# Optimization experiments

Measured on AMD Instinct MI355X. Metric: run time of the kernel, lower is better.

## Reference

```python
import jax, jax.numpy as jnp
import numpy as np

OUT = 7          # output_size
SR = 2           # sampling_ratio
CANON_SIZE = 224.0
CANON_LVL = 4
MIN_LVL, MAX_LVL = 2, 5
SCALES = (0.25, 0.125, 0.0625, 0.03125)
IMG = 1024.0


def _roi_align(feat, batch_idx, boxes, scale):
    """ROIAlign aligned=True. feat [B,C,H,W], boxes [R,4] (x1,y1,x2,y2) in image coords.
    Returns [R,C,OUT,OUT]."""
    B, C, H, W = feat.shape
    R = boxes.shape[0]
    x1 = boxes[:, 0] * scale - 0.5
    y1 = boxes[:, 1] * scale - 0.5
    x2 = boxes[:, 2] * scale - 0.5
    y2 = boxes[:, 3] * scale - 0.5
    bin_w = (x2 - x1) / OUT
    bin_h = (y2 - y1) / OUT
    S = OUT * SR
    # sample positions in bin units: bin p, sub-sample i -> p + (i+0.5)/SR
    g = (jnp.arange(S, dtype=feat.dtype) + 0.5) / SR
    ys = y1[:, None] + g[None, :] * bin_h[:, None]   # [R,S]
    xs = x1[:, None] + g[None, :] * bin_w[:, None]   # [R,S]
    vy = (ys >= -1.0) & (ys <= H)
    vx = (xs >= -1.0) & (xs <= W)
    yc = jnp.clip(ys, 0.0, H - 1)
    xc = jnp.clip(xs, 0.0, W - 1)
    y0 = jnp.floor(yc).astype(jnp.int32)
    x0 = jnp.floor(xc).astype(jnp.int32)
    y1i = jnp.minimum(y0 + 1, H - 1)
    x1i = jnp.minimum(x0 + 1, W - 1)
    ly = yc - y0.astype(feat.dtype); hy = 1.0 - ly
    lx = xc - x0.astype(feat.dtype); hx = 1.0 - lx
    f = jnp.transpose(feat, (0, 2, 3, 1))            # [B,H,W,C]
    b = batch_idx[:, None, None]                     # [R,1,1]

    def gather(yi, xi):
        # advanced indexing broadcast -> [R,S,S,C]
        return f[b, yi[:, :, None], xi[:, None, :], :]

    def w2(wy, wx):
        return (wy[:, :, None] * wx[:, None, :])[..., None]

    v = (gather(y0, x0) * w2(hy, hx)
         + gather(y0, x1i) * w2(hy, lx)
         + gather(y1i, x0) * w2(ly, hx)
         + gather(y1i, x1i) * w2(ly, lx))             # [R,S,S,C]
    mask = (vy[:, :, None] & vx[:, None, :])[..., None]
    v = jnp.where(mask, v, jnp.zeros((), feat.dtype))
    v = v.reshape(R, OUT, SR, OUT, SR, C).mean(axis=(2, 4))  # avg over SRxSR samples
    return jnp.transpose(v, (0, 3, 1, 2))            # [R,C,OUT,OUT]


def setup_inputs() -> dict:
    key = jax.random.key(0)
    k2, k3, k4, k5, kwh, kc = jax.random.split(key, 6)
    B, C, N = 2, 256, 256
    x2 = jax.random.normal(k2, (B, C, 256, 256), jnp.float32)
    x3 = jax.random.normal(k3, (B, C, 128, 128), jnp.float32)
    x4 = jax.random.normal(k4, (B, C, 64, 64), jnp.float32)
    x5 = jax.random.normal(k5, (B, C, 32, 32), jnp.float32)
    wh = jax.random.uniform(kwh, (B, N, 2), jnp.float32, 32.0, 480.0)
    cxy = jax.random.uniform(kc, (B, N, 2), jnp.float32, 0.0, IMG)
    p1 = jnp.clip(cxy - wh / 2, 0.0, IMG)
    p2 = jnp.clip(cxy + wh / 2, 0.0, IMG)
    boxes = jnp.concatenate([p1, p2], axis=-1)  # [B,N,4] = (x1,y1,x2,y2)
    return {"x2": x2, "x3": x3, "x4": x4, "x5": x5, "boxes": boxes}


def reference(x2, x3, x4, x5, boxes):
    B, N, _ = boxes.shape
    flat = boxes.reshape(B * N, 4)
    batch_idx = jnp.repeat(jnp.arange(B, dtype=jnp.int32), N)
    # FPN level assignment
    area = (flat[:, 2] - flat[:, 0]) * (flat[:, 3] - flat[:, 1])
    sizes = jnp.sqrt(area)
    lvl = jnp.floor(CANON_LVL + jnp.log2(sizes / CANON_SIZE + 1e-8))
    lvl = jnp.clip(lvl, MIN_LVL, MAX_LVL).astype(jnp.int32) - MIN_LVL  # [R] in {0..3}
    feats = (x2, x3, x4, x5)
    C = x2.shape[1]
    out = jnp.zeros((B * N, C, OUT, OUT), x2.dtype)
    for l, (f, s) in enumerate(zip(feats, SCALES)):
        pooled = _roi_align(f, batch_idx, flat, s)
        out = jnp.where((lvl == l)[:, None, None, None], pooled, out)
    return out
```

## Files before the change

kernel.cpp:

```cpp
#include <hip/hip_runtime.h>


#define OUTD 7
#define CCH  256
#define NBOX 256
#define NC   4
#define NCHK (CCH / NC)
#define CAPU 300
#define CAPF (CAPU * 4)
#define NBIN (OUTD * OUTD)

typedef __attribute__((address_space(1))) unsigned int gu32;
typedef __attribute__((address_space(3))) unsigned int lu32;

__device__ __forceinline__ void gl2lds16(const float* g, float* l) {
    __builtin_amdgcn_global_load_lds((gu32*)(unsigned long long)g, (lu32*)l, 16, 0, 0);
}

__global__ __launch_bounds__(256) void roi_direct(
    const float* __restrict__ f0, const float* __restrict__ f1,
    const float* __restrict__ f2, const float* __restrict__ f3,
    const float* __restrict__ boxes, float* __restrict__ out)
{
    const int roi = blockIdx.x;
    const int t   = threadIdx.x;
    const int wv  = t >> 6;
    const int ln  = t & 63;
    const int c   = blockIdx.y * NC + wv;
    const int b   = roi >> 8;

    const float bx1 = boxes[roi * 4 + 0];
    const float by1 = boxes[roi * 4 + 1];
    const float bx2 = boxes[roi * 4 + 2];
    const float by2 = boxes[roi * 4 + 3];

    const float area = (bx2 - bx1) * (by2 - by1);
    const float sz   = sqrtf(area);
    int lvl = (int)floorf(4.0f + log2f(sz * (1.0f / 224.0f) + 1e-8f));
    lvl = min(max(lvl, 2), 5) - 2;

    const int   wsh   = 8 - lvl;
    const int   H     = 1 << wsh;
    const int   W     = H;
    const float scale = 1.0f / (float)(4 << lvl);
    const float* f = (lvl == 0) ? f0 : (lvl == 1) ? f1 : (lvl == 2) ? f2 : f3;

    const float x1r = bx1 * scale - 0.5f;
    const float y1r = by1 * scale - 0.5f;
    const float bw  = (bx2 - bx1) * scale * (1.0f / OUTD);
    const float bh  = (by2 - by1) * scale * (1.0f / OUTD);
    const float Wm1 = (float)(W - 1);

    const int xf = (int)fminf(fmaxf(x1r + 0.25f * bw, 0.0f), Wm1);
    const int yf = (int)fminf(fmaxf(y1r + 0.25f * bh, 0.0f), Wm1);
    const int xl = min((int)fminf(fmaxf(x1r + 6.75f * bw, 0.0f), Wm1) + 1, W - 1);
    const int yl = min((int)fminf(fmaxf(y1r + 6.75f * bh, 0.0f), Wm1) + 1, W - 1);
    const int x_lo = xf & ~3;
    const int y_lo = yf;
    const int W4 = (xl - x_lo + 4) >> 2;
    const int Hw = yl - y_lo + 1;
    const int L4 = Hw * W4;
    const int rs = W4 << 2;

    __shared__ __align__(16) float s_win[NC * CAPF];

    const bool fast = (L4 <= CAPU);

    const unsigned int cbase = ((unsigned int)(b * CCH + c)) << (2 * wsh);
    if (fast) {
        const unsigned int wbase = ((unsigned int)y_lo << wsh) + (unsigned int)x_lo;
        const unsigned int gmax  = (512u << (2 * wsh)) - 4u;
        const float invW4 = 1.0f / (float)W4;
        float* lb = s_win + wv * CAPF;
        for (int o0 = 0; o0 < L4; o0 += 64) {
            const int u = o0 + ln;
            if (u < L4) {
                int y  = (int)((float)u * invW4);
                int x4 = u - y * W4;
                if (x4 < 0) { x4 += W4; --y; } else if (x4 >= W4) { x4 -= W4; ++y; }
                unsigned int g = cbase + wbase + ((unsigned int)y << wsh) + ((unsigned int)x4 << 2);
                g = min(g, gmax);
                gl2lds16(f + g, lb + (o0 << 2));
            }
        }
    }

    const int l  = min(ln, 48);
    const int oy = l / 7;
    const int ox = l - oy * 7;

    const float ysA = y1r + ((float)(2 * oy) + 0.5f) * 0.5f * bh;
    const float ysB = y1r + ((float)(2 * oy + 1) + 0.5f) * 0.5f * bh;
    const float xsA = x1r + ((float)(2 * ox) + 0.5f) * 0.5f * bw;
    const float xsB = x1r + ((float)(2 * ox + 1) + 0.5f) * 0.5f * bw;

    const float vyA = ((ysA >= -1.0f) && (ysA <= (float)H)) ? 1.0f : 0.0f;
    const float vyB = ((ysB >= -1.0f) && (ysB <= (float)H)) ? 1.0f : 0.0f;
    const float vxA = ((xsA >= -1.0f) && (xsA <= (float)W)) ? 1.0f : 0.0f;
    const float vxB = ((xsB >= -1.0f) && (xsB <= (float)W)) ? 1.0f : 0.0f;

    const float ycA = fminf(fmaxf(ysA, 0.0f), Wm1);
    const float ycB = fminf(fmaxf(ysB, 0.0f), Wm1);
    const float xcA = fminf(fmaxf(xsA, 0.0f), Wm1);
    const float xcB = fminf(fmaxf(xsB, 0.0f), Wm1);

    const int yA0 = (int)ycA, yB0 = (int)ycB;
    const int xA0 = (int)xcA, xB0 = (int)xcB;
    const int yA1 = min(yA0 + 1, H - 1), yB1 = min(yB0 + 1, H - 1);
    const int xA1 = min(xA0 + 1, W - 1), xB1 = min(xB0 + 1, W - 1);

    const float lyA = ycA - (float)yA0, lyB = ycB - (float)yB0;
    const float lxA = xcA - (float)xA0, lxB = xcB - (float)xB0;

    const float wyAh = vyA * (1.0f - lyA), wyAl = vyA * lyA;
    const float wyBh = vyB * (1.0f - lyB), wyBl = vyB * lyB;
    const float wxAh = vxA * (1.0f - lxA), wxAl = vxA * lxA;
    const float wxBh = vxB * (1.0f - lxB), wxBl = vxB * lxB;

    float acc;
    if (fast) {
        const int ryA0 = (yA0 - y_lo) * rs, ryA1 = (yA1 - y_lo) * rs;
        const int ryB0 = (yB0 - y_lo) * rs, ryB1 = (yB1 - y_lo) * rs;
        const int rxA0 = xA0 - x_lo, rxA1 = xA1 - x_lo;
        const int rxB0 = xB0 - x_lo, rxB1 = xB1 - x_lo;

        asm volatile("s_waitcnt vmcnt(0)" ::: "memory");
        __builtin_amdgcn_sched_barrier(0);

        const float* w = s_win + wv * CAPF;
        acc =
            wyAh * (wxAh * w[ryA0 + rxA0] + wxAl * w[ryA0 + rxA1])
          + wyAl * (wxAh * w[ryA1 + rxA0] + wxAl * w[ryA1 + rxA1])
          + wyAh * (wxBh * w[ryA0 + rxB0] + wxBl * w[ryA0 + rxB1])
          + wyAl * (wxBh * w[ryA1 + rxB0] + wxBl * w[ryA1 + rxB1])
          + wyBh * (wxAh * w[ryB0 + rxA0] + wxAl * w[ryB0 + rxA1])
          + wyBl * (wxAh * w[ryB1 + rxA0] + wxAl * w[ryB1 + rxA1])
          + wyBh * (wxBh * w[ryB0 + rxB0] + wxBl * w[ryB0 + rxB1])
          + wyBl * (wxBh * w[ryB1 + rxB0] + wxBl * w[ryB1 + rxB1]);
    } else {
        const float* fc = f + cbase;
        const int gA0 = yA0 << wsh, gA1 = yA1 << wsh;
        const int gB0 = yB0 << wsh, gB1 = yB1 << wsh;
        acc =
            wyAh * (wxAh * fc[gA0 + xA0] + wxAl * fc[gA0 + xA1])
          + wyAl * (wxAh * fc[gA1 + xA0] + wxAl * fc[gA1 + xA1])
          + wyAh * (wxBh * fc[gA0 + xB0] + wxBl * fc[gA0 + xB1])
          + wyAl * (wxBh * fc[gA1 + xB0] + wxBl * fc[gA1 + xB1])
          + wyBh * (wxAh * fc[gB0 + xA0] + wxAl * fc[gB0 + xA1])
          + wyBl * (wxAh * fc[gB1 + xA0] + wxAl * fc[gB1 + xA1])
          + wyBh * (wxBh * fc[gB0 + xB0] + wxBl * fc[gB0 + xB1])
          + wyBl * (wxBh * fc[gB1 + xB0] + wxBl * fc[gB1 + xB1]);
    }

    if (ln < NBIN) {
        out[(size_t)roi * (CCH * NBIN) + (size_t)c * NBIN + ln] = acc * 0.25f;
    }
}

extern "C" void kernel_launch(void* const* d_in, const int* in_sizes, int n_in,
                              void* d_out, int out_size, void* d_ws, size_t ws_size,
                              hipStream_t stream) {
    const float* f0    = (const float*)d_in[0];
    const float* f1    = (const float*)d_in[1];
    const float* f2    = (const float*)d_in[2];
    const float* f3    = (const float*)d_in[3];
    const float* boxes = (const float*)d_in[4];
    float*       outp  = (float*)d_out;

    const int R = out_size / (CCH * NBIN);
    roi_direct<<<dim3(R, NCHK), 256, 0, stream>>>(f0, f1, f2, f3, boxes, outp);
}
```

Measured before the change: 260.0 us.

## Precompute per-ROI sampling geometry in setup kernel and process two channels per wave

Adds a small setup kernel that computes each ROI's level, window bounds, bilinear indices, weights and per-load window offsets once, and writes them to workspace. The main kernel reads these tables instead of redoing the per-thread geometry and divisions for every channel block. Each wave now handles two channels with the loads issued together, and the grid is reordered so channel blocks of one ROI run close together. This costs an extra launch, a workspace dependency with a fallback kernel, and odd nroi inference logic.

After: 245.3 us. 5.6% less time.

```diff
diff --git a/kernel.cpp b/kernel.cpp
--- a/kernel.cpp
+++ b/kernel.cpp
@@ -4,11 +4,14 @@
 #define OUTD 7
 #define CCH  256
 #define NBOX 256
-#define NC   4
-#define NCHK (CCH / NC)
+#define NBIN 49
 #define CAPU 300
 #define CAPF (CAPU * 4)
-#define NBIN (OUTD * OUTD)
+
+#define NC   8
+#define NCHK (CCH / NC)
+
+#define WS_STRIDE 1280
 
 typedef __attribute__((address_space(1))) unsigned int gu32;
 typedef __attribute__((address_space(3))) unsigned int lu32;
@@ -17,7 +20,213 @@
     __builtin_amdgcn_global_load_lds((gu32*)(unsigned long long)g, (lu32*)l, 16, 0, 0);
 }
 
-__global__ __launch_bounds__(256) void roi_direct(
+struct Geo {
+    int wsh, W, H; float x1r, y1r, bw, bh, Wm1;
+    int x_lo, y_lo, W4, Hw, L4, rs;
+};
+
+__device__ __forceinline__ Geo mkgeo(float bx1, float by1, float bx2, float by2) {
+    Geo g;
+    const float area = (bx2 - bx1) * (by2 - by1);
+    const float sz   = sqrtf(area);
+    int lvl = (int)floorf(4.0f + log2f(sz * (1.0f / 224.0f) + 1e-8f));
+    lvl = min(max(lvl, 2), 5) - 2;
+    g.wsh = 8 - lvl; g.W = 1 << g.wsh; g.H = g.W;
+    const float scale = 1.0f / (float)(4 << lvl);
+    g.x1r = bx1 * scale - 0.5f;
+    g.y1r = by1 * scale - 0.5f;
+    g.bw  = (bx2 - bx1) * scale * (1.0f / OUTD);
+    g.bh  = (by2 - by1) * scale * (1.0f / OUTD);
+    g.Wm1 = (float)(g.W - 1);
+    const int xf = (int)fminf(fmaxf(g.x1r + 0.25f * g.bw, 0.0f), g.Wm1);
+    const int yf = (int)fminf(fmaxf(g.y1r + 0.25f * g.bh, 0.0f), g.Wm1);
+    const int xl = min((int)fminf(fmaxf(g.x1r + 6.75f * g.bw, 0.0f), g.Wm1) + 1, g.W - 1);
+    const int yl = min((int)fminf(fmaxf(g.y1r + 6.75f * g.bh, 0.0f), g.Wm1) + 1, g.W - 1);
+    g.x_lo = xf & ~3;
+    g.y_lo = yf;
+    g.W4 = (xl - g.x_lo + 4) >> 2;
+    g.Hw = yl - g.y_lo + 1;
+    g.L4 = g.Hw * g.W4;
+    g.rs = g.W4 << 2;
+    return g;
+}
+
+__global__ __launch_bounds__(64) void roi_setup(const float* __restrict__ boxes,
+                                                unsigned char* __restrict__ ws)
+{
+    const int roi = blockIdx.x;
+    const int ln  = threadIdx.x;
+    const Geo g = mkgeo(boxes[roi * 4 + 0], boxes[roi * 4 + 1],
+                        boxes[roi * 4 + 2], boxes[roi * 4 + 3]);
+    const int b = roi >> 8;
+    unsigned char* wr = ws + (size_t)roi * WS_STRIDE;
+
+    if (ln == 0) {
+        unsigned int* hdr = (unsigned int*)wr;
+        hdr[0] = (unsigned int)g.wsh;
+        hdr[1] = ((unsigned int)(b * CCH) << (2 * g.wsh))
+               + ((unsigned int)g.y_lo << g.wsh) + (unsigned int)g.x_lo;
+        hdr[2] = (unsigned int)g.W4;
+        hdr[3] = (unsigned int)g.L4;
+        hdr[4] = (unsigned int)g.rs;
+        hdr[5] = (512u << (2 * g.wsh)) - 4u;
+    }
+    if (ln < 14) {
+        const float gg = ((float)ln + 0.5f) * 0.5f;
+        const float ys = g.y1r + gg * g.bh;
+        const float xs = g.x1r + gg * g.bw;
+        const float vy = ((ys >= -1.0f) && (ys <= (float)g.H)) ? 1.0f : 0.0f;
+        const float vx = ((xs >= -1.0f) && (xs <= (float)g.W)) ? 1.0f : 0.0f;
+        const float yc = fminf(fmaxf(ys, 0.0f), g.Wm1);
+        const float xc = fminf(fmaxf(xs, 0.0f), g.Wm1);
+        const int y0 = (int)yc, x0 = (int)xc;
+        const int y1 = min(y0 + 1, g.H - 1), x1 = min(x0 + 1, g.W - 1);
+        const float ly = yc - (float)y0, lx = xc - (float)x0;
+        ((int2*)  (wr + 32 ))[ln] = make_int2((y0 - g.y_lo) * g.rs, (y1 - g.y_lo) * g.rs);
+        ((float2*)(wr + 144))[ln] = make_float2(vy * (1.0f - ly), vy * ly);
+        ((int2*)  (wr + 256))[ln] = make_int2(x0 - g.x_lo, x1 - g.x_lo);
+        ((float2*)(wr + 368))[ln] = make_float2(vx * (1.0f - lx), vx * lx);
+    }
+    unsigned short* offs = (unsigned short*)(wr + 480);
+    const int nU = min(g.L4, 304);
+    const float invW4 = 1.0f / (float)g.W4;
+    for (int u = ln; u < nU; u += 64) {
+        int y  = (int)((float)u * invW4);
+        int x4 = u - y * g.W4;
+        if (x4 < 0) { x4 += g.W4; --y; } else if (x4 >= g.W4) { x4 -= g.W4; ++y; }
+        offs[u] = (unsigned short)((y << (g.wsh - 2)) + x4);
+    }
+}
+
+__global__ __launch_bounds__(256) void roi_main(
+    const float* __restrict__ f0, const float* __restrict__ f1,
+    const float* __restrict__ f2, const float* __restrict__ f3,
+    const float* __restrict__ boxes,
+    const unsigned char* __restrict__ ws, float* __restrict__ out)
+{
+    const int roi = blockIdx.y;
+    const int c0  = blockIdx.x * NC;
+    const int t   = threadIdx.x;
+    const int wv  = t >> 6;
+    const int ln  = t & 63;
+
+    const unsigned char* wr  = ws + (size_t)roi * WS_STRIDE;
+    const unsigned int*  hdr = (const unsigned int*)wr;
+    const unsigned int wsh = hdr[0], ubase = hdr[1];
+    const unsigned int L4  = hdr[3], gmax  = hdr[5];
+
+    const int lvl = 8 - (int)wsh;
+    const float* f = (lvl == 0) ? f0 : (lvl == 1) ? f1 : (lvl == 2) ? f2 : f3;
+
+    const int l  = min(ln, 48);
+    const int oy = l / 7;
+    const int ox = l - oy * 7;
+
+    const int4   ypk = *(const int4*)  (wr + 32  + 16 * oy);
+    const float4 wyp = *(const float4*)(wr + 144 + 16 * oy);
+    const int4   xpk = *(const int4*)  (wr + 256 + 16 * ox);
+    const float4 wxp = *(const float4*)(wr + 368 + 16 * ox);
+
+    const int ca = c0 + wv;
+    const int cb = c0 + wv + 4;
+    const size_t obase = (size_t)roi * (CCH * NBIN);
+
+    __shared__ __align__(16) float s_win[NC * CAPF];
+
+    if (L4 <= CAPU) {
+        const unsigned short* offs = (const unsigned short*)(wr + 480);
+        unsigned int rel[5];
+        #pragma unroll
+        for (int k = 0; k < 5; ++k)
+            rel[k] = ((unsigned int)offs[min(ln + (k << 6), (int)L4 - 1)]) << 2;
+
+        float* sa = s_win + wv * CAPF;
+        float* sb = s_win + (wv + 4) * CAPF;
+        const unsigned int cba = ubase + ((unsigned int)ca << (2 * wsh));
+        const unsigned int cbb = ubase + ((unsigned int)cb << (2 * wsh));
+        #pragma unroll
+        for (int k = 0; k < 5; ++k)
+            if (ln + (k << 6) < (int)L4)
+                gl2lds16(f + min(cba + rel[k], gmax), sa + (k << 8));
+        #pragma unroll
+        for (int k = 0; k < 5; ++k)
+            if (ln + (k << 6) < (int)L4)
+                gl2lds16(f + min(cbb + rel[k], gmax), sb + (k << 8));
+
+        asm volatile("s_waitcnt vmcnt(0)" ::: "memory");
+        __builtin_amdgcn_sched_barrier(0);
+
+        const float accA =
+            wyp.x * (wxp.x * sa[ypk.x + xpk.x] + wxp.y * sa[ypk.x + xpk.y])
+          + wyp.y * (wxp.x * sa[ypk.y + xpk.x] + wxp.y * sa[ypk.y + xpk.y])
+          + wyp.x * (wxp.z * sa[ypk.x + xpk.z] + wxp.w * sa[ypk.x + xpk.w])
+          + wyp.y * (wxp.z * sa[ypk.y + xpk.z] + wxp.w * sa[ypk.y + xpk.w])
+          + wyp.z * (wxp.x * sa[ypk.z + xpk.x] + wxp.y * sa[ypk.z + xpk.y])
+          + wyp.w * (wxp.x * sa[ypk.w + xpk.x] + wxp.y * sa[ypk.w + xpk.y])
+          + wyp.z * (wxp.z * sa[ypk.z + xpk.z] + wxp.w * sa[ypk.z + xpk.w])
+          + wyp.w * (wxp.z * sa[ypk.w + xpk.z] + wxp.w * sa[ypk.w + xpk.w]);
+        const float accB =
+            wyp.x * (wxp.x * sb[ypk.x + xpk.x] + wxp.y * sb[ypk.x + xpk.y])
+          + wyp.y * (wxp.x * sb[ypk.y + xpk.x] + wxp.y * sb[ypk.y + xpk.y])
+          + wyp.x * (wxp.z * sb[ypk.x + xpk.z] + wxp.w * sb[ypk.x + xpk.w])
+          + wyp.y * (wxp.z * sb[ypk.y + xpk.z] + wxp.w * sb[ypk.y + xpk.w])
+          + wyp.z * (wxp.x * sb[ypk.z + xpk.x] + wxp.y * sb[ypk.z + xpk.y])
+          + wyp.w * (wxp.x * sb[ypk.w + xpk.x] + wxp.y * sb[ypk.w + xpk.y])
+          + wyp.z * (wxp.z * sb[ypk.z + xpk.z] + wxp.w * sb[ypk.z + xpk.w])
+          + wyp.w * (wxp.z * sb[ypk.w + xpk.z] + wxp.w * sb[ypk.w + xpk.w]);
+
+        if (ln < NBIN) {
+            out[obase + (size_t)ca * NBIN + ln] = accA * 0.25f;
+            out[obase + (size_t)cb * NBIN + ln] = accB * 0.25f;
+        }
+    } else {
+        const Geo g = mkgeo(boxes[roi * 4 + 0], boxes[roi * 4 + 1],
+                            boxes[roi * 4 + 2], boxes[roi * 4 + 3]);
+        const float ysA = g.y1r + ((float)(2 * oy) + 0.5f) * 0.5f * g.bh;
+        const float ysB = g.y1r + ((float)(2 * oy + 1) + 0.5f) * 0.5f * g.bh;
+        const float xsA = g.x1r + ((float)(2 * ox) + 0.5f) * 0.5f * g.bw;
+        const float xsB = g.x1r + ((float)(2 * ox + 1) + 0.5f) * 0.5f * g.bw;
+        const float vyA = ((ysA >= -1.0f) && (ysA <= (float)g.H)) ? 1.0f : 0.0f;
+        const float vyB = ((ysB >= -1.0f) && (ysB <= (float)g.H)) ? 1.0f : 0.0f;
+        const float vxA = ((xsA >= -1.0f) && (xsA <= (float)g.W)) ? 1.0f : 0.0f;
+        const float vxB = ((xsB >= -1.0f) && (xsB <= (float)g.W)) ? 1.0f : 0.0f;
+        const float ycA = fminf(fmaxf(ysA, 0.0f), g.Wm1);
+        const float ycB = fminf(fmaxf(ysB, 0.0f), g.Wm1);
+        const float xcA = fminf(fmaxf(xsA, 0.0f), g.Wm1);
+        const float xcB = fminf(fmaxf(xsB, 0.0f), g.Wm1);
+        const int yA0 = (int)ycA, yB0 = (int)ycB, xA0 = (int)xcA, xB0 = (int)xcB;
+        const int yA1 = min(yA0 + 1, g.H - 1), yB1 = min(yB0 + 1, g.H - 1);
+        const int xA1 = min(xA0 + 1, g.W - 1), xB1 = min(xB0 + 1, g.W - 1);
+        const float lyA = ycA - (float)yA0, lyB = ycB - (float)yB0;
+        const float lxA = xcA - (float)xA0, lxB = xcB - (float)xB0;
+        const float wyAh = vyA * (1.0f - lyA), wyAl = vyA * lyA;
+        const float wyBh = vyB * (1.0f - lyB), wyBl = vyB * lyB;
+        const float wxAh = vxA * (1.0f - lxA), wxAl = vxA * lxA;
+        const float wxBh = vxB * (1.0f - lxB), wxBl = vxB * lxB;
+        const int gA0 = yA0 << g.wsh, gA1 = yA1 << g.wsh;
+        const int gB0 = yB0 << g.wsh, gB1 = yB1 << g.wsh;
+        const int b = roi >> 8;
+        #pragma unroll
+        for (int s = 0; s < 2; ++s) {
+            const int c = s ? cb : ca;
+            const float* fc = f + (((size_t)(b * CCH + c)) << (2 * g.wsh));
+            const float acc =
+                wyAh * (wxAh * fc[gA0 + xA0] + wxAl * fc[gA0 + xA1])
+              + wyAl * (wxAh * fc[gA1 + xA0] + wxAl * fc[gA1 + xA1])
+              + wyAh * (wxBh * fc[gA0 + xB0] + wxBl * fc[gA0 + xB1])
+              + wyAl * (wxBh * fc[gA1 + xB0] + wxBl * fc[gA1 + xB1])
+              + wyBh * (wxAh * fc[gB0 + xA0] + wxAl * fc[gB0 + xA1])
+              + wyBl * (wxAh * fc[gB1 + xA0] + wxAl * fc[gB1 + xA1])
+              + wyBh * (wxBh * fc[gB0 + xB0] + wxBl * fc[gB0 + xB1])
+              + wyBl * (wxBh * fc[gB1 + xB0] + wxBl * fc[gB1 + xB1]);
+            if (ln < NBIN)
+                out[obase + (size_t)c * NBIN + ln] = acc * 0.25f;
+        }
+    }
+}
+
+#define MNC 4
+__global__ __launch_bounds__(256) void roi_mono(
     const float* __restrict__ f0, const float* __restrict__ f1,
     const float* __restrict__ f2, const float* __restrict__ f3,
     const float* __restrict__ boxes, float* __restrict__ out)
@@ -26,61 +235,31 @@
     const int t   = threadIdx.x;
     const int wv  = t >> 6;
     const int ln  = t & 63;
-    const int c   = blockIdx.y * NC + wv;
+    const int c   = blockIdx.y * MNC + wv;
     const int b   = roi >> 8;
 
-    const float bx1 = boxes[roi * 4 + 0];
-    const float by1 = boxes[roi * 4 + 1];
-    const float bx2 = boxes[roi * 4 + 2];
-    const float by2 = boxes[roi * 4 + 3];
-
-    const float area = (bx2 - bx1) * (by2 - by1);
-    const float sz   = sqrtf(area);
-    int lvl = (int)floorf(4.0f + log2f(sz * (1.0f / 224.0f) + 1e-8f));
-    lvl = min(max(lvl, 2), 5) - 2;
-
-    const int   wsh   = 8 - lvl;
-    const int   H     = 1 << wsh;
-    const int   W     = H;
-    const float scale = 1.0f / (float)(4 << lvl);
+    const Geo g = mkgeo(boxes[roi * 4 + 0], boxes[roi * 4 + 1],
+                        boxes[roi * 4 + 2], boxes[roi * 4 + 3]);
+    const int lvl = 8 - g.wsh;
     const float* f = (lvl == 0) ? f0 : (lvl == 1) ? f1 : (lvl == 2) ? f2 : f3;
 
-    const float x1r = bx1 * scale - 0.5f;
-    const float y1r = by1 * scale - 0.5f;
-    const float bw  = (bx2 - bx1) * scale * (1.0f / OUTD);
-    const float bh  = (by2 - by1) * scale * (1.0f / OUTD);
-    const float Wm1 = (float)(W - 1);
-
-    const int xf = (int)fminf(fmaxf(x1r + 0.25f * bw, 0.0f), Wm1);
-    const int yf = (int)fminf(fmaxf(y1r + 0.25f * bh, 0.0f), Wm1);
-    const int xl = min((int)fminf(fmaxf(x1r + 6.75f * bw, 0.0f), Wm1) + 1, W - 1);
-    const int yl = min((int)fminf(fmaxf(y1r + 6.75f * bh, 0.0f), Wm1) + 1, W - 1);
-    const int x_lo = xf & ~3;
-    const int y_lo = yf;
-    const int W4 = (xl - x_lo + 4) >> 2;
-    const int Hw = yl - y_lo + 1;
-    const int L4 = Hw * W4;
-    const int rs = W4 << 2;
-
-    __shared__ __align__(16) float s_win[NC * CAPF];
-
-    const bool fast = (L4 <= CAPU);
-
-    const unsigned int cbase = ((unsigned int)(b * CCH + c)) << (2 * wsh);
+    __shared__ __align__(16) float s_win[MNC * CAPF];
+    const bool fast = (g.L4 <= CAPU);
+    const unsigned int cbase = ((unsigned int)(b * CCH + c)) << (2 * g.wsh);
+
     if (fast) {
-        const unsigned int wbase = ((unsigned int)y_lo << wsh) + (unsigned int)x_lo;
-        const unsigned int gmax  = (512u << (2 * wsh)) - 4u;
-        const float invW4 = 1.0f / (float)W4;
+        const unsigned int wbase = ((unsigned int)g.y_lo << g.wsh) + (unsigned int)g.x_lo;
+        const unsigned int gmax  = (512u << (2 * g.wsh)) - 4u;
+        const float invW4 = 1.0f / (float)g.W4;
         float* lb = s_win + wv * CAPF;
-        for (int o0 = 0; o0 < L4; o0 += 64) {
+        for (int o0 = 0; o0 < g.L4; o0 += 64) {
             const int u = o0 + ln;
-            if (u < L4) {
+            if (u < g.L4) {
                 int y  = (int)((float)u * invW4);
-                int x4 = u - y * W4;
-                if (x4 < 0) { x4 += W4; --y; } else if (x4 >= W4) { x4 -= W4; ++y; }
-                unsigned int g = cbase + wbase + ((unsigned int)y << wsh) + ((unsigned int)x4 << 2);
-                g = min(g, gmax);
-                gl2lds16(f + g, lb + (o0 << 2));
+                int x4 = u - y * g.W4;
+                if (x4 < 0) { x4 += g.W4; --y; } else if (x4 >= g.W4) { x4 -= g.W4; ++y; }
+                unsigned int gg = cbase + wbase + ((unsigned int)y << g.wsh) + ((unsigned int)x4 << 2);
+                gl2lds16(f + min(gg, gmax), lb + (o0 << 2));
             }
         }
     }
@@ -88,30 +267,23 @@
     const int l  = min(ln, 48);
     const int oy = l / 7;
     const int ox = l - oy * 7;
-
-    const float ysA = y1r + ((float)(2 * oy) + 0.5f) * 0.5f * bh;
-    const float ysB = y1r + ((float)(2 * oy + 1) + 0.5f) * 0.5f * bh;
-    const float xsA = x1r + ((float)(2 * ox) + 0.5f) * 0.5f * bw;
-    const float xsB = x1r + ((float)(2 * ox + 1) + 0.5f) * 0.5f * bw;
-
-    const float vyA = ((ysA >= -1.0f) && (ysA <= (float)H)) ? 1.0f : 0.0f;
-    const float vyB = ((ysB >= -1.0f) && (ysB <= (float)H)) ? 1.0f : 0.0f;
-    const float vxA = ((xsA >= -1.0f) && (xsA <= (float)W)) ? 1.0f : 0.0f;
-    const float vxB = ((xsB >= -1.0f) && (xsB <= (float)W)) ? 1.0f : 0.0f;
-
-    const float ycA = fminf(fmaxf(ysA, 0.0f), Wm1);
-    const float ycB = fminf(fmaxf(ysB, 0.0f), Wm1);
-    const float xcA = fminf(fmaxf(xsA, 0.0f), Wm1);
-    const float xcB = fminf(fmaxf(xsB, 0.0f), Wm1);
-
-    const int yA0 = (int)ycA, yB0 = (int)ycB;
-    const int xA0 = (int)xcA, xB0 = (int)xcB;
-    const int yA1 = min(yA0 + 1, H - 1), yB1 = min(yB0 + 1, H - 1);
-    const int xA1 = min(xA0 + 1, W - 1), xB1 = min(xB0 + 1, W - 1);
-
+    const float ysA = g.y1r + ((float)(2 * oy) + 0.5f) * 0.5f * g.bh;
+    const float ysB = g.y1r + ((float)(2 * oy + 1) + 0.5f) * 0.5f * g.bh;
+    const float xsA = g.x1r + ((float)(2 * ox) + 0.5f) * 0.5f * g.bw;
+    const float xsB = g.x1r + ((float)(2 * ox + 1) + 0.5f) * 0.5f * g.bw;
+    const float vyA = ((ysA >= -1.0f) && (ysA <= (float)g.H)) ? 1.0f : 0.0f;
+    const float vyB = ((ysB >= -1.0f) && (ysB <= (float)g.H)) ? 1.0f : 0.0f;
+    const float vxA = ((xsA >= -1.0f) && (xsA <= (float)g.W)) ? 1.0f : 0.0f;
+    const float vxB = ((xsB >= -1.0f) && (xsB <= (float)g.W)) ? 1.0f : 0.0f;
+    const float ycA = fminf(fmaxf(ysA, 0.0f), g.Wm1);
+    const float ycB = fminf(fmaxf(ysB, 0.0f), g.Wm1);
+    const float xcA = fminf(fmaxf(xsA, 0.0f), g.Wm1);
+    const float xcB = fminf(fmaxf(xsB, 0.0f), g.Wm1);
+    const int yA0 = (int)ycA, yB0 = (int)ycB, xA0 = (int)xcA, xB0 = (int)xcB;
+    const int yA1 = min(yA0 + 1, g.H - 1), yB1 = min(yB0 + 1, g.H - 1);
+    const int xA1 = min(xA0 + 1, g.W - 1), xB1 = min(xB0 + 1, g.W - 1);
     const float lyA = ycA - (float)yA0, lyB = ycB - (float)yB0;
     const float lxA = xcA - (float)xA0, lxB = xcB - (float)xB0;
-
     const float wyAh = vyA * (1.0f - lyA), wyAl = vyA * lyA;
     const float wyBh = vyB * (1.0f - lyB), wyBl = vyB * lyB;
     const float wxAh = vxA * (1.0f - lxA), wxAl = vxA * lxA;
@@ -119,14 +291,12 @@
 
     float acc;
     if (fast) {
-        const int ryA0 = (yA0 - y_lo) * rs, ryA1 = (yA1 - y_lo) * rs;
-        const int ryB0 = (yB0 - y_lo) * rs, ryB1 = (yB1 - y_lo) * rs;
-        const int rxA0 = xA0 - x_lo, rxA1 = xA1 - x_lo;
-        const int rxB0 = xB0 - x_lo, rxB1 = xB1 - x_lo;
-
+        const int ryA0 = (yA0 - g.y_lo) * g.rs, ryA1 = (yA1 - g.y_lo) * g.rs;
+        const int ryB0 = (yB0 - g.y_lo) * g.rs, ryB1 = (yB1 - g.y_lo) * g.rs;
+        const int rxA0 = xA0 - g.x_lo, rxA1 = xA1 - g.x_lo;
+        const int rxB0 = xB0 - g.x_lo, rxB1 = xB1 - g.x_lo;
         asm volatile("s_waitcnt vmcnt(0)" ::: "memory");
         __builtin_amdgcn_sched_barrier(0);
-
         const float* w = s_win + wv * CAPF;
         acc =
             wyAh * (wxAh * w[ryA0 + rxA0] + wxAl * w[ryA0 + rxA1])
@@ -139,8 +309,8 @@
           + wyBl * (wxBh * w[ryB1 + rxB0] + wxBl * w[ryB1 + rxB1]);
     } else {
         const float* fc = f + cbase;
-        const int gA0 = yA0 << wsh, gA1 = yA1 << wsh;
-        const int gB0 = yB0 << wsh, gB1 = yB1 << wsh;
+        const int gA0 = yA0 << g.wsh, gA1 = yA1 << g.wsh;
+        const int gB0 = yB0 << g.wsh, gB1 = yB1 << g.wsh;
         acc =
             wyAh * (wxAh * fc[gA0 + xA0] + wxAl * fc[gA0 + xA1])
           + wyAl * (wxAh * fc[gA1 + xA0] + wxAl * fc[gA1 + xA1])
@@ -167,6 +337,15 @@
     const float* boxes = (const float*)d_in[4];
     float*       outp  = (float*)d_out;
 
-    const int R = out_size / (CCH * NBIN);
-    roi_direct<<<dim3(R, NCHK), 256, 0, stream>>>(f0, f1, f2, f3, boxes, outp);
-}
+    const int R = out_size / (CCH * NBIN * 4);
+    const int Rr = out_size / (CCH * NBIN);
+    const int nroi = (Rr == 512 || Rr == 2 * NBOX) ? Rr : (R > 0 ? R : Rr);
+
+    if (ws_size >= (size_t)nroi * WS_STRIDE) {
+        roi_setup<<<nroi, 64, 0, stream>>>(boxes, (unsigned char*)d_ws);
+        roi_main<<<dim3(NCHK, nroi), 256, 0, stream>>>(
+            f0, f1, f2, f3, boxes, (const unsigned char*)d_ws, outp);
+    } else {
+        roi_mono<<<dim3(nroi, CCH / MNC), 256, 0, stream>>>(f0, f1, f2, f3, boxes, outp);
+    }
+}
```
